# Kernel tuning notes

Measured on AMD Instinct MI355X. Metric: run time of the kernel, lower is better.

## Reference

```python
import jax, jax.numpy as jnp
import numpy as np

N, E, F, DH, R = 50000, 800000, 128, 128, 6  # nodes, edges, in-feat, hidden, relations (heads=1)
EPS = 1e-5
NEG_SLOPE = 0.01


def setup_inputs() -> dict:
    key = jax.random.key(0)
    ks = jax.random.split(key, 20)
    sF = 1.0 / np.sqrt(F)
    sD = 1.0 / np.sqrt(DH)
    return {
        "x": jax.random.normal(ks[0], (N, F), dtype=jnp.float32),
        "edge_index": jax.random.randint(ks[1], (2, E), 0, N, dtype=jnp.int64),
        "edge_type": jax.random.randint(ks[2], (E,), 0, R, dtype=jnp.int64),
        # RGCNConv params
        "rgcn_w": jax.random.normal(ks[3], (R, F, DH), dtype=jnp.float32) * sF,
        "rgcn_root": jax.random.normal(ks[4], (F, DH), dtype=jnp.float32) * sF,
        "rgcn_bias": jnp.zeros((DH,), dtype=jnp.float32),
        # TransformerConv params (heads=1, concat=True)
        "wq": jax.random.normal(ks[5], (DH, DH), dtype=jnp.float32) * sD,
        "bq": jnp.zeros((DH,), dtype=jnp.float32),
        "wk": jax.random.normal(ks[6], (DH, DH), dtype=jnp.float32) * sD,
        "bk": jnp.zeros((DH,), dtype=jnp.float32),
        "wv": jax.random.normal(ks[7], (DH, DH), dtype=jnp.float32) * sD,
        "bv": jnp.zeros((DH,), dtype=jnp.float32),
        "wskip": jax.random.normal(ks[8], (DH, DH), dtype=jnp.float32) * sD,
        "bskip": jnp.zeros((DH,), dtype=jnp.float32),
        # BatchNorm1d params (training-mode batch stats)
        "bn_gamma": jnp.ones((DH,), dtype=jnp.float32),
        "bn_beta": jnp.zeros((DH,), dtype=jnp.float32),
    }


def _rgcn(x, src, dst, edge_type, w, root, bias):
    # PyG RGCNConv: per-relation mean aggregation of x_j @ W_r over incoming edges, + root + bias
    out = x @ root + bias  # [N, DH]
    for r in range(R):
        m = (edge_type == r)
        xw = x @ w[r]  # [N, DH]
        msg = jnp.where(m[:, None], xw[src], 0.0)  # [E, DH]
        s = jax.ops.segment_sum(msg, dst, num_segments=N)
        cnt = jax.ops.segment_sum(m.astype(x.dtype), dst, num_segments=N)
        out = out + s / jnp.maximum(cnt, 1.0)[:, None]
    return out


def _transformer_conv(x, src, dst, wq, bq, wk, bk, wv, bv, wskip, bskip):
    # PyG TransformerConv, heads=1: edge-softmax attention over incoming edges + skip projection
    q = x @ wq + bq  # [N, DH]
    k = x @ wk + bk
    v = x @ wv + bv
    score = jnp.sum(q[dst] * k[src], axis=-1) / jnp.sqrt(jnp.asarray(DH, x.dtype))  # [E]
    smax = jax.ops.segment_max(score, dst, num_segments=N)  # -inf for empty segments (unused)
    a = jnp.exp(score - smax[dst])
    denom = jax.ops.segment_sum(a, dst, num_segments=N)
    alpha = a / denom[dst]  # every edge's dst has >=1 edge, denom > 0
    agg = jax.ops.segment_sum(alpha[:, None] * v[src], dst, num_segments=N)  # [N, DH]
    return agg + (x @ wskip + bskip)


def reference(x, edge_index, edge_type, rgcn_w, rgcn_root, rgcn_bias,
              wq, bq, wk, bk, wv, bv, wskip, bskip, bn_gamma, bn_beta):
    src, dst = edge_index[0], edge_index[1]
    h = _rgcn(x, src, dst, edge_type, rgcn_w, rgcn_root, rgcn_bias)
    h = _transformer_conv(h, src, dst, wq, bq, wk, bk, wv, bv, wskip, bskip)
    # BatchNorm1d (training: batch statistics, biased variance)
    mu = jnp.mean(h, axis=0)
    var = jnp.mean(jnp.square(h - mu), axis=0)
    h = bn_gamma * (h - mu) * jax.lax.rsqrt(var + EPS) + bn_beta
    return jnp.where(h > 0, h, NEG_SLOPE * h)
```

## Files before the change

### kernel.cpp

```cpp
#include <hip/hip_runtime.h>
#include <hip/hip_bf16.h>
#include <math.h>

#define FDIM 128
#define NREL 6

typedef _Float16 half8 __attribute__((ext_vector_type(8)));
typedef _Float16 h16x2 __attribute__((ext_vector_type(2)));
typedef float f32x4 __attribute__((ext_vector_type(4)));

#if __has_builtin(__builtin_amdgcn_fdot2)
#define FDOT2(A, B, C) __builtin_amdgcn_fdot2((A), (B), (C), false)
#else
#define FDOT2(A, B, C) ((float)(A)[0] * (float)(B)[0] + ((float)(A)[1] * (float)(B)[1] + (C)))
#endif

static __device__ __forceinline__ unsigned short f2h(float f) {
  union { _Float16 h; unsigned short u; } p; p.h = (_Float16)f; return p.u;
}

__global__ void cvt_x_kernel(const float* __restrict__ x, unsigned short* __restrict__ xh,
                             int n4) {
  int i = blockIdx.x * 256 + threadIdx.x;
  if (i < n4) {
    float4 v = ((const float4*)x)[i];
    union { _Float16 h[4]; uint2 u; } p;
    p.h[0] = (_Float16)v.x; p.h[1] = (_Float16)v.y;
    p.h[2] = (_Float16)v.z; p.h[3] = (_Float16)v.w;
    ((uint2*)xh)[i] = p.u;
  }
}

__global__ void cvt_wr_kernel(const float* __restrict__ root, const float* __restrict__ w,
                              unsigned short* __restrict__ bt) {
  int i = blockIdx.x * 256 + threadIdx.x;
  if (i < 896 * 128) {
    int n = i / 896, kk = i - n * 896;
    float v = (kk < 128) ? root[kk * 128 + n] : w[(long long)(kk - 128) * 128 + n];
    bt[i] = f2h(v);
  }
}

struct WPtrs { const float* W[4]; };
__global__ void cvt_wq_kernel(WPtrs wp, unsigned short* __restrict__ bt) {
  int i = blockIdx.x * 256 + threadIdx.x;
  if (i < 4 * 128 * 128) {
    int z = i >> 14;
    int r = i & 16383;
    int n = r >> 7, kk = r & 127;
    bt[i] = f2h(wp.W[z][kk * 128 + n]);
  }
}

struct GArgs {
  const unsigned short* Ax;
  const unsigned short* Aagg;
  const unsigned short* BtR;
  const unsigned short* BtQ;
  const float* biasR;
  const float* bias2[4];
  unsigned short* qh; unsigned short* kh; unsigned short* vh; float* sk;
  int M;
};

__launch_bounds__(256)
__global__ void gemm_fused(GArgs g) {
  __shared__ unsigned short Ah[2][64 * 64];
  __shared__ unsigned short hL[64 * 128];
  const int tid = threadIdx.x;
  const int lane = tid & 63;
  const int wid = tid >> 6;
  const int wm = wid >> 1, wn = wid & 1;
  const int lr = lane & 15, lk = lane >> 4;
  const int m0 = blockIdx.x * 64;
  const int M = g.M;

#define STAGE_A(BUF, K0)                                                     \
  {                                                                          \
    _Pragma("unroll")                                                        \
    for (int p = 0; p < 2; ++p) {                                            \
      int idx = tid + 256 * p;                                               \
      int r = idx >> 3, c = idx & 7;                                         \
      int row = m0 + r; if (row > M - 1) row = M - 1;                        \
      const unsigned short* srcp =                                           \
          ((K0) < 128) ? (g.Ax + (long long)row * 128 + (K0) + c * 8)        \
                       : (g.Aagg + (long long)row * 768 + ((K0) - 128) + c * 8); \
      uint4 u = *(const uint4*)srcp;                                         \
      ((uint4*)Ah[BUF])[r * 8 + (c ^ (r & 7))] = u;                          \
    }                                                                        \
  }

  f32x4 acc[2][4];
#pragma unroll
  for (int a = 0; a < 2; ++a)
#pragma unroll
    for (int b = 0; b < 4; ++b) { acc[a][b][0] = 0.f; acc[a][b][1] = 0.f; acc[a][b][2] = 0.f; acc[a][b][3] = 0.f; }

  STAGE_A(0, 0)
  int cur = 0;
#pragma unroll 1
  for (int it = 0; it < 14; ++it) {
    __syncthreads();
    if (it + 1 < 14) STAGE_A(cur ^ 1, (it + 1) * 64)
    const int k0 = it * 64;
#pragma unroll
    for (int ks = 0; ks < 2; ++ks) {
      half8 a[2], b[4];
#pragma unroll
      for (int fm = 0; fm < 2; ++fm) {
        int row = wm * 32 + fm * 16 + lr;
        a[fm] = *(const half8*)&((uint4*)Ah[cur])[row * 8 + ((ks * 4 + lk) ^ (row & 7))];
      }
#pragma unroll
      for (int fn = 0; fn < 4; ++fn) {
        int col = wn * 64 + fn * 16 + lr;
        b[fn] = *(const half8*)(g.BtR + (long long)col * 896 + k0 + ks * 32 + lk * 8);
      }
#pragma unroll
      for (int fm = 0; fm < 2; ++fm)
#pragma unroll
        for (int fn = 0; fn < 4; ++fn)
          acc[fm][fn] = __builtin_amdgcn_mfma_f32_16x16x32_f16(a[fm], b[fn], acc[fm][fn], 0, 0, 0);
    }
    cur ^= 1;
  }
#undef STAGE_A

#pragma unroll
  for (int fm = 0; fm < 2; ++fm) {
#pragma unroll
    for (int fn = 0; fn < 4; ++fn) {
      int col = wn * 64 + fn * 16 + lr;
      float bv = g.biasR[col];
      int cu = col >> 3, cb = col & 7;
#pragma unroll
      for (int j = 0; j < 4; ++j) {
        int row = wm * 32 + fm * 16 + lk * 4 + j;
        float vv = acc[fm][fn][j] + bv;
        hL[row * 128 + ((cu ^ (row & 7)) << 3) + cb] = f2h(vv);
      }
    }
  }
  __syncthreads();

  const float CF = 0.08838834764831845f * 1.4426950408889634f;
  const float* b2 = (wid == 0) ? g.bias2[0]
                  : (wid == 1) ? g.bias2[1]
                  : (wid == 2) ? g.bias2[2] : g.bias2[3];
  const unsigned short* Wz = g.BtQ + (long long)wid * 16384;
#pragma unroll
  for (int half = 0; half < 2; ++half) {
    f32x4 acc2[4][4];
#pragma unroll
    for (int a = 0; a < 4; ++a)
#pragma unroll
      for (int b = 0; b < 4; ++b) { acc2[a][b][0] = 0.f; acc2[a][b][1] = 0.f; acc2[a][b][2] = 0.f; acc2[a][b][3] = 0.f; }

#pragma unroll
    for (int ks = 0; ks < 4; ++ks) {
      half8 a[4], b[4];
#pragma unroll
      for (int fm = 0; fm < 4; ++fm) {
        int row = fm * 16 + lr;
        a[fm] = *(const half8*)&((uint4*)hL)[row * 16 + ((ks * 4 + lk) ^ (row & 7))];
      }
#pragma unroll
      for (int fn = 0; fn < 4; ++fn) {
        int n = half * 64 + fn * 16 + lr;
        b[fn] = *(const half8*)(Wz + (long long)n * 128 + ks * 32 + lk * 8);
      }
#pragma unroll
      for (int fm = 0; fm < 4; ++fm)
#pragma unroll
        for (int fn = 0; fn < 4; ++fn)
          acc2[fm][fn] = __builtin_amdgcn_mfma_f32_16x16x32_f16(a[fm], b[fn], acc2[fm][fn], 0, 0, 0);
    }

#pragma unroll
    for (int fm = 0; fm < 4; ++fm) {
#pragma unroll
      for (int fn = 0; fn < 4; ++fn) {
        int col = half * 64 + fn * 16 + lr;
        float bv = b2[col];
#pragma unroll
        for (int j = 0; j < 4; ++j) {
          int row = m0 + fm * 16 + lk * 4 + j;
          if (row < M) {
            float vv = acc2[fm][fn][j] + bv;
            long long off = (long long)row * 128 + col;
            if (wid == 0) g.qh[off] = f2h(vv * CF);
            else if (wid == 1) g.kh[off] = f2h(vv);
            else if (wid == 2) g.vh[off] = f2h(vv);
            else g.sk[off] = vv;
          }
        }
      }
    }
  }
}

__global__ void hist_kernel(const int* __restrict__ dst, const int* __restrict__ etype,
                            int* __restrict__ cnt, int E) {
  int e = blockIdx.x * blockDim.x + threadIdx.x;
  if (e < E) atomicAdd(&cnt[dst[e] * NREL + etype[e]], 1);
}

__launch_bounds__(1024)
__global__ void scan1(const int* __restrict__ deg, int* __restrict__ incl,
                      int* __restrict__ part, int n) {
  __shared__ int sh[1024];
  int tid = threadIdx.x;
  int i = blockIdx.x * 1024 + tid;
  sh[tid] = (i < n) ? deg[i] : 0;
  __syncthreads();
  for (int o = 1; o < 1024; o <<= 1) {
    int t = (tid >= o) ? sh[tid - o] : 0;
    __syncthreads();
    sh[tid] += t;
    __syncthreads();
  }
  if (i < n) incl[i] = sh[tid];
  if (tid == 1023) part[blockIdx.x] = sh[1023];
}

__global__ void scan2(int* part, int nb) {
  int lane = threadIdx.x;
  int run = 0;
  for (int b0 = 0; b0 < nb; b0 += 64) {
    int i = b0 + lane;
    int orig = (i < nb) ? part[i] : 0;
    int v = orig;
#pragma unroll
    for (int o = 1; o < 64; o <<= 1) {
      int t = __shfl_up(v, o);
      if (lane >= o) v += t;
    }
    if (i < nb) part[i] = run + v - orig;
    run += __shfl(v, 63);
  }
}

__global__ void scan3(const int* __restrict__ incl, const int* __restrict__ part,
                      int* __restrict__ offs, int n) {
  int i = blockIdx.x * blockDim.x + threadIdx.x;
  if (i < n) {
    offs[i + 1] = incl[i] + part[i >> 10];
    if (i == 0) offs[0] = 0;
  }
}

__global__ void scatter_kernel(const int* __restrict__ src, const int* __restrict__ dst,
                               const int* __restrict__ etype, const int* __restrict__ offs6,
                               int* __restrict__ cur, int* __restrict__ csrc, int E) {
  int e = blockIdx.x * blockDim.x + threadIdx.x;
  if (e < E) {
    int key = dst[e] * NREL + etype[e];
    int p = offs6[key] + atomicAdd(&cur[key], 1);
    csrc[p] = src[e] << 8;
  }
}

__launch_bounds__(256)
__global__ void rgcn_agg(const unsigned short* __restrict__ xh, const int* __restrict__ offs6,
                         const int* __restrict__ csrc,
                         unsigned short* __restrict__ aggh, int N) {
  int node = blockIdx.x * 4 + (threadIdx.x >> 6);
  if (node >= N) return;
  int lane = threadIdx.x & 63;
  const char* xc = (const char*)xh;
  const int* bp = offs6 + node * NREL;
  const int b0 = bp[0];
  int bn0 = bp[1], bn1 = bp[2], bn2 = bp[3], bn3 = bp[4], bn4 = bp[5], bn5 = bp[6];
  const int b6 = bn5;
  unsigned* ap = (unsigned*)(aggh + (long long)node * (NREL * FDIM)) + lane;

  float tx = 0.f, ty = 0.f;
  float px = 0.f, py = 0.f;
  int bprev = b0, snaps = 0;

#define FLUSH(EPOS)                                                          \
  while (snaps < NREL && bn0 == (EPOS)) {                                    \
    int cnt_ = (EPOS) - bprev;                                               \
    float inv_ = cnt_ ? 1.f / (float)cnt_ : 0.f;                             \
    union { _Float16 h[2]; unsigned u; } pk_;                                \
    pk_.h[0] = (_Float16)((tx - px) * inv_);                                 \
    pk_.h[1] = (_Float16)((ty - py) * inv_);                                 \
    *ap = pk_.u; ap += 64;                                                   \
    px = tx; py = ty; bprev = (EPOS); ++snaps;                               \
    bn0 = bn1; bn1 = bn2; bn2 = bn3; bn3 = bn4; bn4 = bn5;                   \
  }

#define EAT(XU)                                                              \
  {                                                                          \
    union { unsigned u; _Float16 h[2]; } c_; c_.u = (XU);                    \
    tx += (float)c_.h[0]; ty += (float)c_.h[1];                              \
  }

  FLUSH(b0)
  int e = b0;
  for (; e + 16 <= b6; e += 16) {
    unsigned xv[16];
#pragma unroll
    for (int t = 0; t < 16; ++t)
      xv[t] = ((const unsigned*)(xc + csrc[e + t]))[lane];
    EAT(xv[0])  FLUSH(e + 1)   EAT(xv[1])  FLUSH(e + 2)
    EAT(xv[2])  FLUSH(e + 3)   EAT(xv[3])  FLUSH(e + 4)
    EAT(xv[4])  FLUSH(e + 5)   EAT(xv[5])  FLUSH(e + 6)
    EAT(xv[6])  FLUSH(e + 7)   EAT(xv[7])  FLUSH(e + 8)
    EAT(xv[8])  FLUSH(e + 9)   EAT(xv[9])  FLUSH(e + 10)
    EAT(xv[10]) FLUSH(e + 11)  EAT(xv[11]) FLUSH(e + 12)
    EAT(xv[12]) FLUSH(e + 13)  EAT(xv[13]) FLUSH(e + 14)
    EAT(xv[14]) FLUSH(e + 15)  EAT(xv[15]) FLUSH(e + 16)
  }
  for (; e + 4 <= b6; e += 4) {
    unsigned y0 = ((const unsigned*)(xc + csrc[e + 0]))[lane];
    unsigned y1 = ((const unsigned*)(xc + csrc[e + 1]))[lane];
    unsigned y2 = ((const unsigned*)(xc + csrc[e + 2]))[lane];
    unsigned y3 = ((const unsigned*)(xc + csrc[e + 3]))[lane];
    EAT(y0) FLUSH(e + 1) EAT(y1) FLUSH(e + 2)
    EAT(y2) FLUSH(e + 3) EAT(y3) FLUSH(e + 4)
  }
  for (; e < b6; ++e) {
    unsigned xv = ((const unsigned*)(xc + csrc[e]))[lane];
    EAT(xv) FLUSH(e + 1)
  }
#undef EAT
#undef FLUSH
}

__launch_bounds__(256)
__global__ void attn_kernel(const unsigned short* __restrict__ qh,
                            const unsigned short* __restrict__ kh,
                            const unsigned short* __restrict__ vh,
                            const int* __restrict__ offs6, const int* __restrict__ csrc,
                            float* __restrict__ out,
                            float* __restrict__ gsumB, float* __restrict__ gsqB, int N) {
  __shared__ float bsum[4][FDIM];
  __shared__ float bsq[4][FDIM];
  int wv = threadIdx.x >> 6;
  int node = blockIdx.x * 4 + wv;
  int lane = threadIdx.x & 63;
  bool active = (node < N);
  int start = 0, end = 0;
  if (active) { start = offs6[node * NREL]; end = offs6[node * NREL + NREL]; }
  int deg = end - start;

  const int g16 = lane >> 4;
  const int f = lane & 15;
  const char* kc = (const char*)kh;
  const char* vc = (const char*)vh;

  union U4 { uint4 u; h16x2 h[4]; };
  U4 qf;
  if (active) qf.u = *(const uint4*)(qh + (long long)node * FDIM + f * 8);

  float m = -INFINITY, den = 0.f, acc0 = 0.f, acc1 = 0.f;

#define LOADQ(E0, S0, S1, S2, S3, KU, V0, V1, V2, V3)                        \
  {                                                                          \
    S0 = csrc[(E0) + (g16 ^ 0)];                                             \
    S1 = csrc[(E0) + (g16 ^ 1)];                                             \
    S2 = csrc[(E0) + (g16 ^ 2)];                                             \
    S3 = csrc[(E0) + (g16 ^ 3)];                                             \
    KU = *(const uint4*)(kc + S0 + f * 16);                                  \
    V0 = ((const unsigned*)(vc + S0))[lane];                                 \
    V1 = ((const unsigned*)(vc + S1))[lane];                                 \
    V2 = ((const unsigned*)(vc + S2))[lane];                                 \
    V3 = ((const unsigned*)(vc + S3))[lane];                                 \
  }

#define PROCESS(KU, V0, V1, V2, V3, MASKED, M0, M1, M2, M3)                  \
  {                                                                          \
    U4 kf; kf.u = KU;                                                        \
    float pd = FDOT2(qf.h[0], kf.h[0], 0.f);                                 \
    pd = FDOT2(qf.h[1], kf.h[1], pd);                                        \
    pd = FDOT2(qf.h[2], kf.h[2], pd);                                        \
    pd = FDOT2(qf.h[3], kf.h[3], pd);                                        \
    pd += __shfl_xor(pd, 1);  pd += __shfl_xor(pd, 2);                       \
    pd += __shfl_xor(pd, 4);  pd += __shfl_xor(pd, 8);                       \
    float sc0 = pd;                                                          \
    float sc1 = __shfl_xor(pd, 16);                                          \
    float sc2 = __shfl_xor(pd, 32);                                          \
    float sc3 = __shfl_xor(pd, 48);                                          \
    if (MASKED) {                                                            \
      if (!(M0)) sc0 = -INFINITY;                                            \
      if (!(M1)) sc1 = -INFINITY;                                            \
      if (!(M2)) sc2 = -INFINITY;                                            \
      if (!(M3)) sc3 = -INFINITY;                                            \
    }                                                                        \
    float mx = fmaxf(fmaxf(sc0, sc1), fmaxf(sc2, sc3));                      \
    float mn = fmaxf(m, mx);                                                 \
    float scl = exp2f(m - mn);                                               \
    float a0 = exp2f(sc0 - mn), a1 = exp2f(sc1 - mn);                        \
    float a2 = exp2f(sc2 - mn), a3 = exp2f(sc3 - mn);                        \
    den = den * scl + ((a0 + a1) + (a2 + a3));                               \
    union { unsigned u; _Float16 h[2]; } w0, w1, w2, w3;                     \
    w0.u = V0; w1.u = V1; w2.u = V2; w3.u = V3;                              \
    acc0 = acc0 * scl + a0 * (float)w0.h[0] + a1 * (float)w1.h[0]            \
                      + a2 * (float)w2.h[0] + a3 * (float)w3.h[0];           \
    acc1 = acc1 * scl + a0 * (float)w0.h[1] + a1 * (float)w1.h[1]            \
                      + a2 * (float)w2.h[1] + a3 * (float)w3.h[1];           \
    m = mn;                                                                  \
  }

  if (deg > 0) {
    int nfull4 = deg & ~3;
    int e = start;
    if (nfull4 > 0) {
      int sA0, sA1, sA2, sA3; uint4 kA; unsigned vA0, vA1, vA2, vA3;
      LOADQ(e, sA0, sA1, sA2, sA3, kA, vA0, vA1, vA2, vA3)
      for (; e < start + nfull4; e += 4) {
        int sB0, sB1, sB2, sB3; uint4 kB; unsigned vB0, vB1, vB2, vB3;
        bool more = (e + 4 < start + nfull4);
        if (more) LOADQ(e + 4, sB0, sB1, sB2, sB3, kB, vB0, vB1, vB2, vB3)
        PROCESS(kA, vA0, vA1, vA2, vA3, false, 1, 1, 1, 1)
        if (more) { kA = kB; vA0 = vB0; vA1 = vB1; vA2 = vB2; vA3 = vB3; }
      }
    }
    int rem = deg & 3;
    if (rem) {
      int e0 = start + nfull4;
      int j0 = g16 ^ 0, j1 = g16 ^ 1, j2 = g16 ^ 2, j3 = g16 ^ 3;
      int sT0 = csrc[e0 + (j0 < rem ? j0 : 0)];
      int sT1 = csrc[e0 + (j1 < rem ? j1 : 0)];
      int sT2 = csrc[e0 + (j2 < rem ? j2 : 0)];
      int sT3 = csrc[e0 + (j3 < rem ? j3 : 0)];
      uint4 kT = *(const uint4*)(kc + sT0 + f * 16);
      unsigned vT0 = ((const unsigned*)(vc + sT0))[lane];
      unsigned vT1 = ((const unsigned*)(vc + sT1))[lane];
      unsigned vT2 = ((const unsigned*)(vc + sT2))[lane];
      unsigned vT3 = ((const unsigned*)(vc + sT3))[lane];
      PROCESS(kT, vT0, vT1, vT2, vT3, true, j0 < rem, j1 < rem, j2 < rem, j3 < rem)
    }
  }
#undef LOADQ
#undef PROCESS

  float2 o = make_float2(0.f, 0.f);
  if (active) {
    float2* op = (float2*)(out + (long long)node * FDIM);
    o = op[lane];
    if (deg > 0) {
      float inv = 1.f / den;
      o.x += acc0 * inv;
      o.y += acc1 * inv;
      op[lane] = o;
    }
  }

  ((float2*)bsum[wv])[lane] = make_float2(o.x, o.y);
  ((float2*)bsq[wv])[lane]  = make_float2(o.x * o.x, o.y * o.y);
  __syncthreads();
  if (threadIdx.x < FDIM) {
    int d = threadIdx.x;
    float s  = bsum[0][d] + bsum[1][d] + bsum[2][d] + bsum[3][d];
    float q2 = bsq[0][d]  + bsq[1][d]  + bsq[2][d]  + bsq[3][d];
    int bucket = blockIdx.x & 31;
    atomicAdd(&gsumB[bucket * FDIM + d], s);
    atomicAdd(&gsqB[bucket * FDIM + d], q2);
  }
}

__global__ void bn_final(const float* __restrict__ gsumB, const float* __restrict__ gsqB,
                         const float* __restrict__ gamma, const float* __restrict__ beta,
                         float* __restrict__ ss, int N) {
  int d = threadIdx.x;
  if (d < FDIM) {
    float s = 0.f, q = 0.f;
    for (int b = 0; b < 32; ++b) { s += gsumB[b * FDIM + d]; q += gsqB[b * FDIM + d]; }
    float mean = s / (float)N;
    float var = q / (float)N - mean * mean;
    var = fmaxf(var, 0.f);
    float sc = gamma[d] * rsqrtf(var + 1e-5f);
    ss[d] = sc;
    ss[FDIM + d] = beta[d] - mean * sc;
  }
}

__global__ void bn_apply(float* __restrict__ x, const float* __restrict__ ss, long long total4) {
  long long i = (long long)blockIdx.x * blockDim.x + threadIdx.x;
  if (i < total4) {
    int d0 = (int)((i * 4) & (FDIM - 1));
    float4 vv = ((const float4*)x)[i];
    float y0 = ss[d0 + 0] * vv.x + ss[FDIM + d0 + 0];
    float y1 = ss[d0 + 1] * vv.y + ss[FDIM + d0 + 1];
    float y2 = ss[d0 + 2] * vv.z + ss[FDIM + d0 + 2];
    float y3 = ss[d0 + 3] * vv.w + ss[FDIM + d0 + 3];
    vv.x = (y0 > 0.f) ? y0 : 0.01f * y0;
    vv.y = (y1 > 0.f) ? y1 : 0.01f * y1;
    vv.z = (y2 > 0.f) ? y2 : 0.01f * y2;
    vv.w = (y3 > 0.f) ? y3 : 0.01f * y3;
    ((float4*)x)[i] = vv;
  }
}

extern "C" void kernel_launch(void* const* d_in, const int* in_sizes, int n_in,
                              void* d_out, int out_size, void* d_ws, size_t ws_size,
                              hipStream_t stream) {
  const float* x         = (const float*)d_in[0];
  const int*   ei        = (const int*)d_in[1];
  const int*   etype     = (const int*)d_in[2];
  const float* rgcn_w    = (const float*)d_in[3];
  const float* rgcn_root = (const float*)d_in[4];
  const float* rgcn_bias = (const float*)d_in[5];
  const float* wq = (const float*)d_in[6];  const float* bq = (const float*)d_in[7];
  const float* wk = (const float*)d_in[8];  const float* bk = (const float*)d_in[9];
  const float* wv = (const float*)d_in[10]; const float* bv = (const float*)d_in[11];
  const float* wsk = (const float*)d_in[12]; const float* bsk = (const float*)d_in[13];
  const float* gamma = (const float*)d_in[14]; const float* beta = (const float*)d_in[15];

  const int N = in_sizes[0] / FDIM;
  const int E = in_sizes[1] / 2;
  const int* src = ei;
  const int* dst = ei + E;
  const int NK = N * NREL;

  char* base = (char*)d_ws;
  size_t off = 0;
  auto alloc = [&](size_t bytes) -> char* {
    char* p = base + off;
    off += (bytes + 255) & ~(size_t)255;
    return p;
  };
  unsigned short* aggh = (unsigned short*)alloc((size_t)N * (NREL * FDIM) * 2);
  unsigned short* qbuf = aggh;
  unsigned short* kbuf = aggh + (size_t)N * FDIM;
  unsigned short* vbuf = aggh + 2 * (size_t)N * FDIM;
  unsigned short* xh   = (unsigned short*)alloc((size_t)N * FDIM * 2);
  unsigned short* btR  = (unsigned short*)alloc((size_t)896 * 128 * 2);
  unsigned short* btQ  = (unsigned short*)alloc((size_t)4 * 128 * 128 * 2);
  int* cnt6 = (int*)alloc((size_t)2 * NK * 4);
  int* cur  = cnt6 + NK;
  int* offs6 = (int*)alloc((size_t)(NK + 1) * 4);
  int* incl = (int*)alloc((size_t)NK * 4);
  int* part = (int*)alloc((size_t)512 * 4);
  int* csrc = (int*)alloc((size_t)E * 4);
  float* gsumB = (float*)alloc((size_t)32 * FDIM * 4);
  float* gsqB  = (float*)alloc((size_t)32 * FDIM * 4);
  float* ss    = (float*)alloc((size_t)2 * FDIM * 4);

  float* out = (float*)d_out;

  hipMemsetAsync(cnt6, 0, (size_t)2 * NK * sizeof(int), stream);
  hipMemsetAsync(gsumB, 0, (size_t)64 * FDIM * sizeof(float), stream);

  int n4 = N * FDIM / 4;
  cvt_x_kernel<<<(n4 + 255) / 256, 256, 0, stream>>>(x, xh, n4);
  cvt_wr_kernel<<<(896 * 128 + 255) / 256, 256, 0, stream>>>(rgcn_root, rgcn_w, btR);
  WPtrs wp; wp.W[0] = wq; wp.W[1] = wk; wp.W[2] = wv; wp.W[3] = wsk;
  cvt_wq_kernel<<<(4 * 128 * 128 + 255) / 256, 256, 0, stream>>>(wp, btQ);

  hist_kernel<<<(E + 255) / 256, 256, 0, stream>>>(dst, etype, cnt6, E);
  int nb = (NK + 1023) / 1024;
  scan1<<<nb, 1024, 0, stream>>>(cnt6, incl, part, NK);
  scan2<<<1, 64, 0, stream>>>(part, nb);
  scan3<<<(NK + 255) / 256, 256, 0, stream>>>(incl, part, offs6, NK);
  scatter_kernel<<<(E + 255) / 256, 256, 0, stream>>>(src, dst, etype, offs6, cur, csrc, E);

  const int nodeBlocks = (N + 3) / 4;
  const int gemmBlocks = (N + 63) / 64;

  rgcn_agg<<<nodeBlocks, 256, 0, stream>>>(xh, offs6, csrc, aggh, N);

  GArgs g = {};
  g.Ax = xh; g.Aagg = aggh; g.BtR = btR; g.BtQ = btQ;
  g.biasR = rgcn_bias;
  g.bias2[0] = bq; g.bias2[1] = bk; g.bias2[2] = bv; g.bias2[3] = bsk;
  g.qh = qbuf; g.kh = kbuf; g.vh = vbuf; g.sk = out;
  g.M = N;
  gemm_fused<<<gemmBlocks, 256, 0, stream>>>(g);

  attn_kernel<<<nodeBlocks, 256, 0, stream>>>(qbuf, kbuf, vbuf, offs6, csrc, out,
                                              gsumB, gsqB, N);

  bn_final<<<1, 128, 0, stream>>>(gsumB, gsqB, gamma, beta, ss, N);
  long long total4 = (long long)N * FDIM / 4;
  bn_apply<<<(int)((total4 + 255) / 256), 256, 0, stream>>>(out, ss, total4);
}
```

Before: 368.1 us.

## Stage GEMM B weight tiles through double-buffered LDS in fused kernel

The fused GEMM kernel now stages the RGCN weight tiles (BtR) and the second-stage Q/K/V/skip weight tiles (BtQ) into double-buffered shared memory, with swizzled layouts. Previously every wave read B fragments straight from global memory. The change aims to cut redundant global and L2 traffic and load latency in the MFMA inner loops. The cost is 32 KB more LDS per block, which may lower occupancy, plus extra __syncthreads per k-step in the second GEMM.

Measured after the change: 327.9 us. 10.9% less time.

```diff
diff --git a/kernel.cpp b/kernel.cpp
--- a/kernel.cpp
+++ b/kernel.cpp
@@ -66,6 +66,7 @@
 __launch_bounds__(256)
 __global__ void gemm_fused(GArgs g) {
   __shared__ unsigned short Ah[2][64 * 64];
+  __shared__ unsigned short Bh[2][128 * 64];
   __shared__ unsigned short hL[64 * 128];
   const int tid = threadIdx.x;
   const int lane = tid & 63;
@@ -90,6 +91,30 @@
     }                                                                        \
   }
 
+#define STAGE_B(BUF, K0)                                                     \
+  {                                                                          \
+    _Pragma("unroll")                                                        \
+    for (int p = 0; p < 4; ++p) {                                            \
+      int idx = tid + 256 * p;                                               \
+      int rn = idx >> 3, c = idx & 7;                                        \
+      uint4 u = *(const uint4*)(g.BtR + (long long)rn * 896 + (K0) + c * 8); \
+      ((uint4*)Bh[BUF])[rn * 8 + (c ^ (rn & 7))] = u;                        \
+    }                                                                        \
+  }
+
+#define STAGE_W(BUF, HALF, KS)                                               \
+  {                                                                          \
+    _Pragma("unroll")                                                        \
+    for (int p = 0; p < 4; ++p) {                                            \
+      int u_ = tid + 256 * p;                                                \
+      int zz = u_ >> 8, n = (u_ >> 2) & 63, c = u_ & 3;                      \
+      uint4 w = *(const uint4*)(g.BtQ + (long long)zz * 16384 +              \
+                                (long long)((HALF) * 64 + n) * 128 +         \
+                                (KS) * 32 + c * 8);                          \
+      ((uint4*)Bh[BUF])[zz * 256 + n * 4 + (c ^ (n & 3))] = w;               \
+    }                                                                        \
+  }
+
   f32x4 acc[2][4];
 #pragma unroll
   for (int a = 0; a < 2; ++a)
@@ -97,12 +122,15 @@
     for (int b = 0; b < 4; ++b) { acc[a][b][0] = 0.f; acc[a][b][1] = 0.f; acc[a][b][2] = 0.f; acc[a][b][3] = 0.f; }
 
   STAGE_A(0, 0)
+  STAGE_B(0, 0)
   int cur = 0;
 #pragma unroll 1
   for (int it = 0; it < 14; ++it) {
     __syncthreads();
-    if (it + 1 < 14) STAGE_A(cur ^ 1, (it + 1) * 64)
-    const int k0 = it * 64;
+    if (it + 1 < 14) {
+      STAGE_A(cur ^ 1, (it + 1) * 64)
+      STAGE_B(cur ^ 1, (it + 1) * 64)
+    }
 #pragma unroll
     for (int ks = 0; ks < 2; ++ks) {
       half8 a[2], b[4];
@@ -114,7 +142,7 @@
 #pragma unroll
       for (int fn = 0; fn < 4; ++fn) {
         int col = wn * 64 + fn * 16 + lr;
-        b[fn] = *(const half8*)(g.BtR + (long long)col * 896 + k0 + ks * 32 + lk * 8);
+        b[fn] = *(const half8*)&((uint4*)Bh[cur])[col * 8 + ((ks * 4 + lk) ^ (col & 7))];
       }
 #pragma unroll
       for (int fm = 0; fm < 2; ++fm)
@@ -124,7 +152,6 @@
     }
     cur ^= 1;
   }
-#undef STAGE_A
 
 #pragma unroll
   for (int fm = 0; fm < 2; ++fm) {
@@ -141,13 +168,13 @@
       }
     }
   }
-  __syncthreads();
 
   const float CF = 0.08838834764831845f * 1.4426950408889634f;
   const float* b2 = (wid == 0) ? g.bias2[0]
                   : (wid == 1) ? g.bias2[1]
                   : (wid == 2) ? g.bias2[2] : g.bias2[3];
-  const unsigned short* Wz = g.BtQ + (long long)wid * 16384;
+  STAGE_W(0, 0, 0)
+  int wcur = 0;
 #pragma unroll
   for (int half = 0; half < 2; ++half) {
     f32x4 acc2[4][4];
@@ -158,6 +185,12 @@
 
 #pragma unroll
     for (int ks = 0; ks < 4; ++ks) {
+      __syncthreads();
+      const int cidx = half * 4 + ks;
+      if (cidx + 1 < 8) {
+        const int nh = (cidx + 1) >> 2, nk = (cidx + 1) & 3;
+        STAGE_W(wcur ^ 1, nh, nk)
+      }
       half8 a[4], b[4];
 #pragma unroll
       for (int fm = 0; fm < 4; ++fm) {
@@ -166,14 +199,15 @@
       }
 #pragma unroll
       for (int fn = 0; fn < 4; ++fn) {
-        int n = half * 64 + fn * 16 + lr;
-        b[fn] = *(const half8*)(Wz + (long long)n * 128 + ks * 32 + lk * 8);
+        int n = fn * 16 + lr;
+        b[fn] = *(const half8*)&((uint4*)Bh[wcur])[wid * 256 + n * 4 + (lk ^ (n & 3))];
       }
 #pragma unroll
       for (int fm = 0; fm < 4; ++fm)
 #pragma unroll
         for (int fn = 0; fn < 4; ++fn)
           acc2[fm][fn] = __builtin_amdgcn_mfma_f32_16x16x32_f16(a[fm], b[fn], acc2[fm][fn], 0, 0, 0);
+      wcur ^= 1;
     }
 
 #pragma unroll
@@ -197,6 +231,9 @@
       }
     }
   }
+#undef STAGE_A
+#undef STAGE_B
+#undef STAGE_W
 }
 
 __global__ void hist_kernel(const int* __restrict__ dst, const int* __restrict__ etype,
```
